# Kernel optimization log

Hardware: AMD Instinct MI355X
Metric: run time of the kernel (lower is better)

## Reference

```python
import jax, jax.numpy as jnp
import numpy as np

HID = 64


def setup_inputs() -> dict:
    key = jax.random.key(0)
    k = jax.random.split(key, 7)
    B, T = 4096, 8192
    x = jax.random.normal(k[0], (B, T, 1), dtype=jnp.float32)
    # Kaiming-uniform-ish init scale; exact values irrelevant for correctness baseline
    W_in = jax.random.normal(k[1], (1, HID), dtype=jnp.float32) * 0.5
    b_in = jax.random.normal(k[2], (HID,), dtype=jnp.float32) * 0.1
    W_s = jax.random.normal(k[3], (HID, HID), dtype=jnp.float32) * (1.0 / np.sqrt(HID))
    b_s = jax.random.normal(k[4], (HID,), dtype=jnp.float32) * 0.1
    W_out = jax.random.normal(k[5], (HID, 1), dtype=jnp.float32) * (1.0 / np.sqrt(HID))
    b_out = jax.random.normal(k[6], (1,), dtype=jnp.float32) * 0.1
    return {"x": x, "W_in": W_in, "b_in": b_in, "W_s": W_s, "b_s": b_s,
            "W_out": W_out, "b_out": b_out}


def reference(x, W_in, b_in, W_s, b_s, W_out, b_out):
    B, T, _ = x.shape
    xt = jnp.swapaxes(x, 0, 1)  # [T, B, 1] -> scan over time

    def step(h, x_t):
        # input_proj on [B,1] -> [B,HID]; tiny GEMM per step (the recurrence is sequential)
        inp = x_t @ W_in + b_in
        h = jax.nn.gelu(h @ W_s + b_s + inp, approximate=False)  # torch GELU = exact erf
        return h, None

    h0 = jnp.zeros((B, HID), dtype=x.dtype)
    h_final, _ = jax.lax.scan(step, h0, xt)
    return h_final @ W_out + b_out  # [B, 1]
```

## Files before the change

### kernel.cpp

```cpp
#include <hip/hip_runtime.h>
#include <cstdint>
#include <cstddef>

#define HID 64
#define RPG 16
#define HSTR 72
#define XSTR 68

typedef short bf16x8 __attribute__((ext_vector_type(8)));
typedef float f32x4 __attribute__((ext_vector_type(4)));

__device__ __forceinline__ float fast_gelu(float z) {
    float u = z * 0.70710678118654752f;
    float a = __builtin_fabsf(u);
    float t = __builtin_amdgcn_rcpf(__builtin_fmaf(0.3275911f, a, 1.0f));
    float e = __builtin_amdgcn_exp2f((u * u) * -1.44269504088896f);
    float p =                   1.061405429f;
    p = __builtin_fmaf(p, t, -1.453152027f);
    p = __builtin_fmaf(p, t,  1.421413741f);
    p = __builtin_fmaf(p, t, -0.284496736f);
    p = __builtin_fmaf(p, t,  0.254829592f);
    p = p * t;
    float er = __builtin_fmaf(-p, e, 1.0f);
    er = __builtin_copysignf(er, u);
    float zh = 0.5f * z;
    return __builtin_fmaf(zh, er, zh);
}

__device__ __forceinline__ ushort bf16_hi(float f) {
    return (ushort)(__float_as_uint(f) >> 16);
}
__device__ __forceinline__ float bf16_f(ushort u) {
    return __uint_as_float(((unsigned)u) << 16);
}

#define STEP(RHI, RLO, WHI, WLO, XB, E0, E1) { \
    const bf16x8 Hhi0 = *reinterpret_cast<const bf16x8*>(RHI); \
    const bf16x8 Hhi1 = *reinterpret_cast<const bf16x8*>((RHI) + 32); \
    const bf16x8 Hlo0 = *reinterpret_cast<const bf16x8*>(RLO); \
    const bf16x8 Hlo1 = *reinterpret_cast<const bf16x8*>((RLO) + 32); \
    const f32x4 zz = {0.f, 0.f, 0.f, 0.f}; \
    f32x4 ahh = __builtin_amdgcn_mfma_f32_16x16x32_bf16(Whi0, Hhi0, zz, 0, 0, 0); \
    f32x4 ac1 = __builtin_amdgcn_mfma_f32_16x16x32_bf16(Whi0, Hlo0, zz, 0, 0, 0); \
    f32x4 ac2 = __builtin_amdgcn_mfma_f32_16x16x32_bf16(Wlo0, Hhi0, zz, 0, 0, 0); \
    ahh = __builtin_amdgcn_mfma_f32_16x16x32_bf16(Whi1, Hhi1, ahh, 0, 0, 0); \
    ac1 = __builtin_amdgcn_mfma_f32_16x16x32_bf16(Whi1, Hlo1, ac1, 0, 0, 0); \
    ac2 = __builtin_amdgcn_mfma_f32_16x16x32_bf16(Wlo1, Hhi1, ac2, 0, 0, 0); \
    const float z0 = (ahh[E0] + ac1[E0]) + (ac2[E0] + __builtin_fmaf((XB), win0, cb0)); \
    const float z1 = (ahh[E1] + ac1[E1]) + (ac2[E1] + __builtin_fmaf((XB), win1, cb1)); \
    const float h0 = fast_gelu(z0); \
    const float h1 = fast_gelu(z1); \
    const unsigned hb0 = __float_as_uint(h0), hb1 = __float_as_uint(h1); \
    *(WHI) = (hb0 >> 16) | (hb1 & 0xffff0000u); \
    const float l0 = h0 - __uint_as_float(hb0 & 0xffff0000u); \
    const float l1 = h1 - __uint_as_float(hb1 & 0xffff0000u); \
    *(WLO) = (__float_as_uint(l0) >> 16) | (__float_as_uint(l1) & 0xffff0000u); \
    __syncthreads(); }

#define MAINLOOP(E0, E1) { \
    const float win0 = W_in[cq + E0]; \
    const float win1 = W_in[cq + E1]; \
    const float cb0  = b_in[cq + E0] + b_s[cq + E0]; \
    const float cb1  = b_in[cq + E1] + b_s[cq + E1]; \
    const ushort* const rhiA = &hlds[0][0][rr * HSTR + 8 * q]; \
    const ushort* const rloA = &hlds[0][1][rr * HSTR + 8 * q]; \
    const ushort* const rhiB = &hlds[1][0][rr * HSTR + 8 * q]; \
    const ushort* const rloB = &hlds[1][1][rr * HSTR + 8 * q]; \
    unsigned* const whiA = reinterpret_cast<unsigned*>(&hlds[0][0][rr * HSTR + cq + E0]); \
    unsigned* const wloA = reinterpret_cast<unsigned*>(&hlds[0][1][rr * HSTR + cq + E0]); \
    unsigned* const whiB = reinterpret_cast<unsigned*>(&hlds[1][0][rr * HSTR + cq + E0]); \
    unsigned* const wloB = reinterpret_cast<unsigned*>(&hlds[1][1][rr * HSTR + cq + E0]); \
    for (int tc = 0; tc < nch; ++tc) { \
        const size_t tg = (size_t)tc * 64; \
        xlds[ww][lane]     = x[(size_t)(bA + ww) * (size_t)T + tg + lane]; \
        xlds[ww + 8][lane] = x[(size_t)(bA + ww + 8) * (size_t)T + tg + lane]; \
        __syncthreads(); \
        _Pragma("unroll 1") \
        for (int t4 = 0; t4 < 16; ++t4) { \
            const f32x4 xq = *reinterpret_cast<const f32x4*>(&xlds[rr][t4 * 4]); \
            STEP(rhiA, rloA, whiB, wloB, xq[0], E0, E1) \
            STEP(rhiB, rloB, whiA, wloA, xq[1], E0, E1) \
            STEP(rhiA, rloA, whiB, wloB, xq[2], E0, E1) \
            STEP(rhiB, rloB, whiA, wloA, xq[3], E0, E1) \
        } \
    } }

__global__ __launch_bounds__(512, 2)
void ssm_kernel(const float* __restrict__ x,
                const float* __restrict__ W_in,
                const float* __restrict__ b_in,
                const float* __restrict__ W_s,
                const float* __restrict__ b_s,
                const float* __restrict__ W_out,
                const float* __restrict__ b_out,
                float* __restrict__ out,
                int B, int T) {
    __shared__ ushort hlds[2][2][RPG * HSTR];
    __shared__ float  xlds[RPG][XSTR];

    const int tid  = threadIdx.x;
    const int ww   = tid >> 6;
    const int g    = ww & 3;
    const int hf   = ww >> 2;
    const int lane = tid & 63;
    const int q    = lane >> 4;
    const int rr   = lane & 15;
    const int bA   = blockIdx.x * RPG;
    const int cq   = 16 * g + 4 * q;

    bf16x8 Whi0, Whi1, Wlo0, Wlo1;
    const int wcol = 16 * g + rr;
#pragma unroll
    for (int e = 0; e < 8; ++e) {
        {   const float wf = W_s[(8 * q + e) * HID + wcol];
            const ushort hi = bf16_hi(wf);
            Whi0[e] = (short)hi;
            Wlo0[e] = (short)bf16_hi(wf - bf16_f(hi)); }
        {   const float wf = W_s[(32 + 8 * q + e) * HID + wcol];
            const ushort hi = bf16_hi(wf);
            Whi1[e] = (short)hi;
            Wlo1[e] = (short)bf16_hi(wf - bf16_f(hi)); }
    }
    asm volatile("" : "+v"(Whi0), "+v"(Whi1), "+v"(Wlo0), "+v"(Wlo1));

    {
        ushort* p = &hlds[0][0][0];
        for (int i = tid; i < 2 * RPG * HSTR; i += 512) p[i] = 0;
    }

    const int nch = T >> 6;

    if (hf == 0) { MAINLOOP(0, 1) } else { MAINLOOP(2, 3) }

    if (ww == 0) {
        const int r  = lane >> 2;
        const int p4 = lane & 3;
        const ushort* hp = &hlds[0][0][r * HSTR + p4 * 16];
        const ushort* lp = &hlds[0][1][r * HSTR + p4 * 16];
        float s = 0.f;
#pragma unroll
        for (int j = 0; j < 16; ++j)
            s = __builtin_fmaf(bf16_f(hp[j]) + bf16_f(lp[j]), W_out[p4 * 16 + j], s);
        s += __shfl_xor(s, 1, 64);
        s += __shfl_xor(s, 2, 64);
        if (p4 == 0) out[bA + r] = s + b_out[0];
    }
}

extern "C" void kernel_launch(void* const* d_in, const int* in_sizes, int n_in,
                              void* d_out, int out_size, void* d_ws, size_t ws_size,
                              hipStream_t stream) {
    const float* x     = (const float*)d_in[0];
    const float* W_in  = (const float*)d_in[1];
    const float* b_in  = (const float*)d_in[2];
    const float* W_s   = (const float*)d_in[3];
    const float* b_s   = (const float*)d_in[4];
    const float* W_out = (const float*)d_in[5];
    const float* b_out = (const float*)d_in[6];
    float* out = (float*)d_out;

    const int B = out_size;
    const int T = in_sizes[0] / B;

    const int blocks = B / RPG;
    ssm_kernel<<<blocks, 512, 0, stream>>>(
        x, W_in, b_in, W_s, b_s, W_out, b_out, out, B, T);
}
```

Baseline: 2.641 ms.

## Halve block to 256 threads, each wave computes four outputs per MFMA tile

Removes the duplicated MFMA work in which two half-blocks each computed the same 16x16 tile but kept only two of its four outputs. Each of four waves now consumes all four accumulator elements, packs them with v_perm, and writes 64-bit LDS stores. The x tile is loaded with float4 and the GELU exponent is rescaled to save a multiply. This cuts redundant matrix work and the number of waves per barrier, but doubles the GELU work per thread and may reduce occupancy and latency hiding.

```diff
diff --git a/kernel.cpp b/kernel.cpp
--- a/kernel.cpp
+++ b/kernel.cpp
@@ -14,7 +14,8 @@
     float u = z * 0.70710678118654752f;
     float a = __builtin_fabsf(u);
     float t = __builtin_amdgcn_rcpf(__builtin_fmaf(0.3275911f, a, 1.0f));
-    float e = __builtin_amdgcn_exp2f((u * u) * -1.44269504088896f);
+    float s = u * 1.20112240878645f;
+    float e = __builtin_amdgcn_exp2f(-(s * s));
     float p =                   1.061405429f;
     p = __builtin_fmaf(p, t, -1.453152027f);
     p = __builtin_fmaf(p, t,  1.421413741f);
@@ -34,7 +35,9 @@
     return __uint_as_float(((unsigned)u) << 16);
 }
 
-#define STEP(RHI, RLO, WHI, WLO, XB, E0, E1) { \
+#define PKHI(b_, a_) __builtin_amdgcn_perm((b_), (a_), 0x07060302u)
+
+#define STEP(RHI, RLO, WHI, WLO, XB) { \
     const bf16x8 Hhi0 = *reinterpret_cast<const bf16x8*>(RHI); \
     const bf16x8 Hhi1 = *reinterpret_cast<const bf16x8*>((RHI) + 32); \
     const bf16x8 Hlo0 = *reinterpret_cast<const bf16x8*>(RLO); \
@@ -46,46 +49,27 @@
     ahh = __builtin_amdgcn_mfma_f32_16x16x32_bf16(Whi1, Hhi1, ahh, 0, 0, 0); \
     ac1 = __builtin_amdgcn_mfma_f32_16x16x32_bf16(Whi1, Hlo1, ac1, 0, 0, 0); \
     ac2 = __builtin_amdgcn_mfma_f32_16x16x32_bf16(Wlo1, Hhi1, ac2, 0, 0, 0); \
-    const float z0 = (ahh[E0] + ac1[E0]) + (ac2[E0] + __builtin_fmaf((XB), win0, cb0)); \
-    const float z1 = (ahh[E1] + ac1[E1]) + (ac2[E1] + __builtin_fmaf((XB), win1, cb1)); \
+    const float z0 = (ahh[0] + ac1[0]) + (ac2[0] + __builtin_fmaf((XB), win0, cb0)); \
+    const float z1 = (ahh[1] + ac1[1]) + (ac2[1] + __builtin_fmaf((XB), win1, cb1)); \
+    const float z2 = (ahh[2] + ac1[2]) + (ac2[2] + __builtin_fmaf((XB), win2, cb2)); \
+    const float z3 = (ahh[3] + ac1[3]) + (ac2[3] + __builtin_fmaf((XB), win3, cb3)); \
     const float h0 = fast_gelu(z0); \
     const float h1 = fast_gelu(z1); \
+    const float h2 = fast_gelu(z2); \
+    const float h3 = fast_gelu(z3); \
     const unsigned hb0 = __float_as_uint(h0), hb1 = __float_as_uint(h1); \
-    *(WHI) = (hb0 >> 16) | (hb1 & 0xffff0000u); \
-    const float l0 = h0 - __uint_as_float(hb0 & 0xffff0000u); \
-    const float l1 = h1 - __uint_as_float(hb1 & 0xffff0000u); \
-    *(WLO) = (__float_as_uint(l0) >> 16) | (__float_as_uint(l1) & 0xffff0000u); \
+    const unsigned hb2 = __float_as_uint(h2), hb3 = __float_as_uint(h3); \
+    uint2 hpk; hpk.x = PKHI(hb1, hb0); hpk.y = PKHI(hb3, hb2); \
+    *(WHI) = hpk; \
+    const unsigned lb0 = __float_as_uint(h0 - __uint_as_float(hb0 & 0xffff0000u)); \
+    const unsigned lb1 = __float_as_uint(h1 - __uint_as_float(hb1 & 0xffff0000u)); \
+    const unsigned lb2 = __float_as_uint(h2 - __uint_as_float(hb2 & 0xffff0000u)); \
+    const unsigned lb3 = __float_as_uint(h3 - __uint_as_float(hb3 & 0xffff0000u)); \
+    uint2 lpk; lpk.x = PKHI(lb1, lb0); lpk.y = PKHI(lb3, lb2); \
+    *(WLO) = lpk; \
     __syncthreads(); }
 
-#define MAINLOOP(E0, E1) { \
-    const float win0 = W_in[cq + E0]; \
-    const float win1 = W_in[cq + E1]; \
-    const float cb0  = b_in[cq + E0] + b_s[cq + E0]; \
-    const float cb1  = b_in[cq + E1] + b_s[cq + E1]; \
-    const ushort* const rhiA = &hlds[0][0][rr * HSTR + 8 * q]; \
-    const ushort* const rloA = &hlds[0][1][rr * HSTR + 8 * q]; \
-    const ushort* const rhiB = &hlds[1][0][rr * HSTR + 8 * q]; \
-    const ushort* const rloB = &hlds[1][1][rr * HSTR + 8 * q]; \
-    unsigned* const whiA = reinterpret_cast<unsigned*>(&hlds[0][0][rr * HSTR + cq + E0]); \
-    unsigned* const wloA = reinterpret_cast<unsigned*>(&hlds[0][1][rr * HSTR + cq + E0]); \
-    unsigned* const whiB = reinterpret_cast<unsigned*>(&hlds[1][0][rr * HSTR + cq + E0]); \
-    unsigned* const wloB = reinterpret_cast<unsigned*>(&hlds[1][1][rr * HSTR + cq + E0]); \
-    for (int tc = 0; tc < nch; ++tc) { \
-        const size_t tg = (size_t)tc * 64; \
-        xlds[ww][lane]     = x[(size_t)(bA + ww) * (size_t)T + tg + lane]; \
-        xlds[ww + 8][lane] = x[(size_t)(bA + ww + 8) * (size_t)T + tg + lane]; \
-        __syncthreads(); \
-        _Pragma("unroll 1") \
-        for (int t4 = 0; t4 < 16; ++t4) { \
-            const f32x4 xq = *reinterpret_cast<const f32x4*>(&xlds[rr][t4 * 4]); \
-            STEP(rhiA, rloA, whiB, wloB, xq[0], E0, E1) \
-            STEP(rhiB, rloB, whiA, wloA, xq[1], E0, E1) \
-            STEP(rhiA, rloA, whiB, wloB, xq[2], E0, E1) \
-            STEP(rhiB, rloB, whiA, wloA, xq[3], E0, E1) \
-        } \
-    } }
-
-__global__ __launch_bounds__(512, 2)
+__global__ __launch_bounds__(256, 1)
 void ssm_kernel(const float* __restrict__ x,
                 const float* __restrict__ W_in,
                 const float* __restrict__ b_in,
@@ -99,14 +83,14 @@
     __shared__ float  xlds[RPG][XSTR];
 
     const int tid  = threadIdx.x;
-    const int ww   = tid >> 6;
-    const int g    = ww & 3;
-    const int hf   = ww >> 2;
+    const int g    = tid >> 6;
     const int lane = tid & 63;
     const int q    = lane >> 4;
     const int rr   = lane & 15;
     const int bA   = blockIdx.x * RPG;
     const int cq   = 16 * g + 4 * q;
+
+    if (bA >= B) return;
 
     bf16x8 Whi0, Whi1, Wlo0, Wlo1;
     const int wcol = 16 * g + rr;
@@ -123,16 +107,50 @@
     }
     asm volatile("" : "+v"(Whi0), "+v"(Whi1), "+v"(Wlo0), "+v"(Wlo1));
 
+    const float win0 = W_in[cq + 0], win1 = W_in[cq + 1];
+    const float win2 = W_in[cq + 2], win3 = W_in[cq + 3];
+    const float cb0 = b_in[cq + 0] + b_s[cq + 0];
+    const float cb1 = b_in[cq + 1] + b_s[cq + 1];
+    const float cb2 = b_in[cq + 2] + b_s[cq + 2];
+    const float cb3 = b_in[cq + 3] + b_s[cq + 3];
+
     {
         ushort* p = &hlds[0][0][0];
-        for (int i = tid; i < 2 * RPG * HSTR; i += 512) p[i] = 0;
+        for (int i = tid; i < 2 * RPG * HSTR; i += 256) p[i] = 0;
     }
+
+    const ushort* const rhiA = &hlds[0][0][rr * HSTR + 8 * q];
+    const ushort* const rloA = &hlds[0][1][rr * HSTR + 8 * q];
+    const ushort* const rhiB = &hlds[1][0][rr * HSTR + 8 * q];
+    const ushort* const rloB = &hlds[1][1][rr * HSTR + 8 * q];
+    uint2* const whiA = reinterpret_cast<uint2*>(&hlds[0][0][rr * HSTR + cq]);
+    uint2* const wloA = reinterpret_cast<uint2*>(&hlds[0][1][rr * HSTR + cq]);
+    uint2* const whiB = reinterpret_cast<uint2*>(&hlds[1][0][rr * HSTR + cq]);
+    uint2* const wloB = reinterpret_cast<uint2*>(&hlds[1][1][rr * HSTR + cq]);
 
     const int nch = T >> 6;
 
-    if (hf == 0) { MAINLOOP(0, 1) } else { MAINLOOP(2, 3) }
+    for (int tc = 0; tc < nch; ++tc) {
+        {
+            const int row = tid >> 4;
+            const int ch  = tid & 15;
+            const float4 xg = *reinterpret_cast<const float4*>(
+                &x[(size_t)(bA + row) * (size_t)T + (size_t)(tc * 64 + ch * 4)]);
+            *reinterpret_cast<float4*>(&xlds[row][ch * 4]) = xg;
+        }
+        __syncthreads();
 
-    if (ww == 0) {
+#pragma unroll 1
+        for (int t4 = 0; t4 < 16; ++t4) {
+            const f32x4 xq = *reinterpret_cast<const f32x4*>(&xlds[rr][t4 * 4]);
+            STEP(rhiA, rloA, whiB, wloB, xq[0])
+            STEP(rhiB, rloB, whiA, wloA, xq[1])
+            STEP(rhiA, rloA, whiB, wloB, xq[2])
+            STEP(rhiB, rloB, whiA, wloA, xq[3])
+        }
+    }
+
+    if (g == 0) {
         const int r  = lane >> 2;
         const int p4 = lane & 3;
         const ushort* hp = &hlds[0][0][r * HSTR + p4 * 16];
@@ -163,6 +181,6 @@
     const int T = in_sizes[0] / B;
 
     const int blocks = B / RPG;
-    ssm_kernel<<<blocks, 512, 0, stream>>>(
+    ssm_kernel<<<blocks, 256, 0, stream>>>(
         x, W_in, b_in, W_s, b_s, W_out, b_out, out, B, T);
 }
```

After: 2.896 ms. 9.6% more time.

## Split recurrent matvec K across wave halves and exchange partial sums through LDS

Applied to the files above, without the earlier changes.

Each pair of waves now splits the 64-wide reduction of the hidden-state matvec. Each wave issues three MFMAs over its 32-element K half instead of six chained MFMAs over the full K. The partial sums are swapped through a new LDS buffer, which adds one extra __syncthreads per time step. The input projection and bias are folded into the MFMA accumulator, bf16 hi/lo packing uses v_perm, and x is loaded as float2. The intent is to shorten the serial per-step dependency chain, at the cost of doubling barriers per step.

```diff
diff --git a/kernel.cpp b/kernel.cpp
--- a/kernel.cpp
+++ b/kernel.cpp
@@ -14,7 +14,8 @@
     float u = z * 0.70710678118654752f;
     float a = __builtin_fabsf(u);
     float t = __builtin_amdgcn_rcpf(__builtin_fmaf(0.3275911f, a, 1.0f));
-    float e = __builtin_amdgcn_exp2f((u * u) * -1.44269504088896f);
+    float s = u * 1.20112240878645f;
+    float e = __builtin_amdgcn_exp2f(-(s * s));
     float p =                   1.061405429f;
     p = __builtin_fmaf(p, t, -1.453152027f);
     p = __builtin_fmaf(p, t,  1.421413741f);
@@ -34,54 +35,53 @@
     return __uint_as_float(((unsigned)u) << 16);
 }
 
-#define STEP(RHI, RLO, WHI, WLO, XB, E0, E1) { \
-    const bf16x8 Hhi0 = *reinterpret_cast<const bf16x8*>(RHI); \
-    const bf16x8 Hhi1 = *reinterpret_cast<const bf16x8*>((RHI) + 32); \
-    const bf16x8 Hlo0 = *reinterpret_cast<const bf16x8*>(RLO); \
-    const bf16x8 Hlo1 = *reinterpret_cast<const bf16x8*>((RLO) + 32); \
+#define PKHI(b_, a_) __builtin_amdgcn_perm((b_), (a_), 0x07060302u)
+
+#define STEP(RHI, RLO, WHI, WLO, XB, BIASED, K0, K1, S0, S1) { \
+    const bf16x8 Hhi = *reinterpret_cast<const bf16x8*>(RHI); \
+    const bf16x8 Hlo = *reinterpret_cast<const bf16x8*>(RLO); \
+    f32x4 ci; \
+    ci[0] = (BIASED) ? __builtin_fmaf((XB), win0, cb0) : 0.f; \
+    ci[1] = (BIASED) ? __builtin_fmaf((XB), win1, cb1) : 0.f; \
+    ci[2] = (BIASED) ? __builtin_fmaf((XB), win2, cb2) : 0.f; \
+    ci[3] = (BIASED) ? __builtin_fmaf((XB), win3, cb3) : 0.f; \
     const f32x4 zz = {0.f, 0.f, 0.f, 0.f}; \
-    f32x4 ahh = __builtin_amdgcn_mfma_f32_16x16x32_bf16(Whi0, Hhi0, zz, 0, 0, 0); \
-    f32x4 ac1 = __builtin_amdgcn_mfma_f32_16x16x32_bf16(Whi0, Hlo0, zz, 0, 0, 0); \
-    f32x4 ac2 = __builtin_amdgcn_mfma_f32_16x16x32_bf16(Wlo0, Hhi0, zz, 0, 0, 0); \
-    ahh = __builtin_amdgcn_mfma_f32_16x16x32_bf16(Whi1, Hhi1, ahh, 0, 0, 0); \
-    ac1 = __builtin_amdgcn_mfma_f32_16x16x32_bf16(Whi1, Hlo1, ac1, 0, 0, 0); \
-    ac2 = __builtin_amdgcn_mfma_f32_16x16x32_bf16(Wlo1, Hhi1, ac2, 0, 0, 0); \
-    const float z0 = (ahh[E0] + ac1[E0]) + (ac2[E0] + __builtin_fmaf((XB), win0, cb0)); \
-    const float z1 = (ahh[E1] + ac1[E1]) + (ac2[E1] + __builtin_fmaf((XB), win1, cb1)); \
+    const f32x4 ahh = __builtin_amdgcn_mfma_f32_16x16x32_bf16(Whi, Hhi, ci, 0, 0, 0); \
+    const f32x4 ac1 = __builtin_amdgcn_mfma_f32_16x16x32_bf16(Whi, Hlo, zz, 0, 0, 0); \
+    const f32x4 ac2 = __builtin_amdgcn_mfma_f32_16x16x32_bf16(Wlo, Hhi, zz, 0, 0, 0); \
+    const f32x4 ps = (ahh + ac1) + ac2; \
+    float2 snd; snd.x = ps[S0]; snd.y = ps[S1]; \
+    *xw = snd; \
+    __syncthreads(); \
+    const float2 rc = *xr; \
+    const float z0 = ps[K0] + rc.x; \
+    const float z1 = ps[K1] + rc.y; \
     const float h0 = fast_gelu(z0); \
     const float h1 = fast_gelu(z1); \
     const unsigned hb0 = __float_as_uint(h0), hb1 = __float_as_uint(h1); \
-    *(WHI) = (hb0 >> 16) | (hb1 & 0xffff0000u); \
-    const float l0 = h0 - __uint_as_float(hb0 & 0xffff0000u); \
-    const float l1 = h1 - __uint_as_float(hb1 & 0xffff0000u); \
-    *(WLO) = (__float_as_uint(l0) >> 16) | (__float_as_uint(l1) & 0xffff0000u); \
+    *(WHI) = PKHI(hb1, hb0); \
+    const unsigned lb0 = __float_as_uint(h0 - __uint_as_float(hb0 & 0xffff0000u)); \
+    const unsigned lb1 = __float_as_uint(h1 - __uint_as_float(hb1 & 0xffff0000u)); \
+    *(WLO) = PKHI(lb1, lb0); \
     __syncthreads(); }
 
-#define MAINLOOP(E0, E1) { \
-    const float win0 = W_in[cq + E0]; \
-    const float win1 = W_in[cq + E1]; \
-    const float cb0  = b_in[cq + E0] + b_s[cq + E0]; \
-    const float cb1  = b_in[cq + E1] + b_s[cq + E1]; \
-    const ushort* const rhiA = &hlds[0][0][rr * HSTR + 8 * q]; \
-    const ushort* const rloA = &hlds[0][1][rr * HSTR + 8 * q]; \
-    const ushort* const rhiB = &hlds[1][0][rr * HSTR + 8 * q]; \
-    const ushort* const rloB = &hlds[1][1][rr * HSTR + 8 * q]; \
-    unsigned* const whiA = reinterpret_cast<unsigned*>(&hlds[0][0][rr * HSTR + cq + E0]); \
-    unsigned* const wloA = reinterpret_cast<unsigned*>(&hlds[0][1][rr * HSTR + cq + E0]); \
-    unsigned* const whiB = reinterpret_cast<unsigned*>(&hlds[1][0][rr * HSTR + cq + E0]); \
-    unsigned* const wloB = reinterpret_cast<unsigned*>(&hlds[1][1][rr * HSTR + cq + E0]); \
+#define MAINLOOP(BIASED, K0, K1, S0, S1) { \
     for (int tc = 0; tc < nch; ++tc) { \
-        const size_t tg = (size_t)tc * 64; \
-        xlds[ww][lane]     = x[(size_t)(bA + ww) * (size_t)T + tg + lane]; \
-        xlds[ww + 8][lane] = x[(size_t)(bA + ww + 8) * (size_t)T + tg + lane]; \
+        { \
+            const int row = tid >> 5;         \
+            const int ch  = tid & 31;         \
+            const float2 xg = *reinterpret_cast<const float2*>( \
+                &x[(size_t)(bA + row) * (size_t)T + (size_t)(tc * 64 + ch * 2)]); \
+            *reinterpret_cast<float2*>(&xlds[row][ch * 2]) = xg; \
+        } \
         __syncthreads(); \
         _Pragma("unroll 1") \
         for (int t4 = 0; t4 < 16; ++t4) { \
             const f32x4 xq = *reinterpret_cast<const f32x4*>(&xlds[rr][t4 * 4]); \
-            STEP(rhiA, rloA, whiB, wloB, xq[0], E0, E1) \
-            STEP(rhiB, rloB, whiA, wloA, xq[1], E0, E1) \
-            STEP(rhiA, rloA, whiB, wloB, xq[2], E0, E1) \
-            STEP(rhiB, rloB, whiA, wloA, xq[3], E0, E1) \
+            STEP(rhiA, rloA, whiB, wloB, xq[0], BIASED, K0, K1, S0, S1) \
+            STEP(rhiB, rloB, whiA, wloA, xq[1], BIASED, K0, K1, S0, S1) \
+            STEP(rhiA, rloA, whiB, wloB, xq[2], BIASED, K0, K1, S0, S1) \
+            STEP(rhiB, rloB, whiA, wloA, xq[3], BIASED, K0, K1, S0, S1) \
         } \
     } }
 
@@ -97,6 +97,7 @@
                 int B, int T) {
     __shared__ ushort hlds[2][2][RPG * HSTR];
     __shared__ float  xlds[RPG][XSTR];
+    __shared__ float  xch[8][64][2];
 
     const int tid  = threadIdx.x;
     const int ww   = tid >> 6;
@@ -108,29 +109,45 @@
     const int bA   = blockIdx.x * RPG;
     const int cq   = 16 * g + 4 * q;
 
-    bf16x8 Whi0, Whi1, Wlo0, Wlo1;
+    if (bA >= B) return;
+
+    bf16x8 Whi, Wlo;
     const int wcol = 16 * g + rr;
 #pragma unroll
     for (int e = 0; e < 8; ++e) {
-        {   const float wf = W_s[(8 * q + e) * HID + wcol];
-            const ushort hi = bf16_hi(wf);
-            Whi0[e] = (short)hi;
-            Wlo0[e] = (short)bf16_hi(wf - bf16_f(hi)); }
-        {   const float wf = W_s[(32 + 8 * q + e) * HID + wcol];
-            const ushort hi = bf16_hi(wf);
-            Whi1[e] = (short)hi;
-            Wlo1[e] = (short)bf16_hi(wf - bf16_f(hi)); }
+        const float wf = W_s[(32 * hf + 8 * q + e) * HID + wcol];
+        const ushort hi = bf16_hi(wf);
+        Whi[e] = (short)hi;
+        Wlo[e] = (short)bf16_hi(wf - bf16_f(hi));
     }
-    asm volatile("" : "+v"(Whi0), "+v"(Whi1), "+v"(Wlo0), "+v"(Wlo1));
+    asm volatile("" : "+v"(Whi), "+v"(Wlo));
+
+    const float win0 = W_in[cq + 0], win1 = W_in[cq + 1];
+    const float win2 = W_in[cq + 2], win3 = W_in[cq + 3];
+    const float cb0 = b_in[cq + 0] + b_s[cq + 0];
+    const float cb1 = b_in[cq + 1] + b_s[cq + 1];
+    const float cb2 = b_in[cq + 2] + b_s[cq + 2];
+    const float cb3 = b_in[cq + 3] + b_s[cq + 3];
 
     {
         ushort* p = &hlds[0][0][0];
-        for (int i = tid; i < 2 * RPG * HSTR; i += 512) p[i] = 0;
+        for (int i = tid; i < 2 * 2 * RPG * HSTR; i += 512) p[i] = 0;
     }
+
+    const ushort* const rhiA = &hlds[0][0][rr * HSTR + 32 * hf + 8 * q];
+    const ushort* const rloA = &hlds[0][1][rr * HSTR + 32 * hf + 8 * q];
+    const ushort* const rhiB = &hlds[1][0][rr * HSTR + 32 * hf + 8 * q];
+    const ushort* const rloB = &hlds[1][1][rr * HSTR + 32 * hf + 8 * q];
+    unsigned* const whiA = reinterpret_cast<unsigned*>(&hlds[0][0][rr * HSTR + cq + 2 * hf]);
+    unsigned* const wloA = reinterpret_cast<unsigned*>(&hlds[0][1][rr * HSTR + cq + 2 * hf]);
+    unsigned* const whiB = reinterpret_cast<unsigned*>(&hlds[1][0][rr * HSTR + cq + 2 * hf]);
+    unsigned* const wloB = reinterpret_cast<unsigned*>(&hlds[1][1][rr * HSTR + cq + 2 * hf]);
+    float2* const xw = reinterpret_cast<float2*>(&xch[ww][lane][0]);
+    const float2* const xr = reinterpret_cast<const float2*>(&xch[ww ^ 4][lane][0]);
 
     const int nch = T >> 6;
 
-    if (hf == 0) { MAINLOOP(0, 1) } else { MAINLOOP(2, 3) }
+    if (hf == 0) { MAINLOOP(1, 0, 1, 2, 3) } else { MAINLOOP(0, 2, 3, 0, 1) }
 
     if (ww == 0) {
         const int r  = lane >> 2;
```

New measurement: 3.090 ms. 1.17x slower.

## Interleave hi/lo hidden rows with XOR swizzle and fold input term into MFMA

Applied to the files above, without the earlier changes.

Changes the LDS hidden-state layout so that each row stores hi and lo bf16 halves contiguously (144 ushorts per row), with XOR-swizzled 8-element slots to avoid bank conflicts on the MFMA operand reads and the packed writes. The input projection plus bias is now passed as the MFMA accumulator init rather than added afterwards. The bf16 packing uses v_perm, the x chunk load uses float2, and the GELU exp2 argument is computed with one fewer multiply. The aim is fewer LDS bank conflicts and fewer VALU ops in the serial per-step critical path, at the cost of extra index arithmetic for the swizzle.

```diff
diff --git a/kernel.cpp b/kernel.cpp
--- a/kernel.cpp
+++ b/kernel.cpp
@@ -4,7 +4,7 @@
 
 #define HID 64
 #define RPG 16
-#define HSTR 72
+#define ROWU 144
 #define XSTR 68
 
 typedef short bf16x8 __attribute__((ext_vector_type(8)));
@@ -14,7 +14,8 @@
     float u = z * 0.70710678118654752f;
     float a = __builtin_fabsf(u);
     float t = __builtin_amdgcn_rcpf(__builtin_fmaf(0.3275911f, a, 1.0f));
-    float e = __builtin_amdgcn_exp2f((u * u) * -1.44269504088896f);
+    float s = u * 1.20112240878645f;
+    float e = __builtin_amdgcn_exp2f(-(s * s));
     float p =                   1.061405429f;
     p = __builtin_fmaf(p, t, -1.453152027f);
     p = __builtin_fmaf(p, t,  1.421413741f);
@@ -34,27 +35,32 @@
     return __uint_as_float(((unsigned)u) << 16);
 }
 
-#define STEP(RHI, RLO, WHI, WLO, XB, E0, E1) { \
-    const bf16x8 Hhi0 = *reinterpret_cast<const bf16x8*>(RHI); \
-    const bf16x8 Hhi1 = *reinterpret_cast<const bf16x8*>((RHI) + 32); \
-    const bf16x8 Hlo0 = *reinterpret_cast<const bf16x8*>(RLO); \
-    const bf16x8 Hlo1 = *reinterpret_cast<const bf16x8*>((RLO) + 32); \
+#define PKHI(b_, a_) __builtin_amdgcn_perm((b_), (a_), 0x07060302u)
+
+#define STEP(RA0, RA1, WHI, WLO, XB, E0, E1) { \
+    const bf16x8 Hhi0 = *reinterpret_cast<const bf16x8*>(RA0); \
+    const bf16x8 Hlo0 = *reinterpret_cast<const bf16x8*>((RA0) + 64); \
+    const bf16x8 Hhi1 = *reinterpret_cast<const bf16x8*>(RA1); \
+    const bf16x8 Hlo1 = *reinterpret_cast<const bf16x8*>((RA1) + 64); \
+    f32x4 ci = {0.f, 0.f, 0.f, 0.f}; \
+    ci[E0] = __builtin_fmaf((XB), win0, cb0); \
+    ci[E1] = __builtin_fmaf((XB), win1, cb1); \
     const f32x4 zz = {0.f, 0.f, 0.f, 0.f}; \
     f32x4 ahh = __builtin_amdgcn_mfma_f32_16x16x32_bf16(Whi0, Hhi0, zz, 0, 0, 0); \
-    f32x4 ac1 = __builtin_amdgcn_mfma_f32_16x16x32_bf16(Whi0, Hlo0, zz, 0, 0, 0); \
+    f32x4 ac1 = __builtin_amdgcn_mfma_f32_16x16x32_bf16(Whi0, Hlo0, ci, 0, 0, 0); \
     f32x4 ac2 = __builtin_amdgcn_mfma_f32_16x16x32_bf16(Wlo0, Hhi0, zz, 0, 0, 0); \
     ahh = __builtin_amdgcn_mfma_f32_16x16x32_bf16(Whi1, Hhi1, ahh, 0, 0, 0); \
     ac1 = __builtin_amdgcn_mfma_f32_16x16x32_bf16(Whi1, Hlo1, ac1, 0, 0, 0); \
     ac2 = __builtin_amdgcn_mfma_f32_16x16x32_bf16(Wlo1, Hhi1, ac2, 0, 0, 0); \
-    const float z0 = (ahh[E0] + ac1[E0]) + (ac2[E0] + __builtin_fmaf((XB), win0, cb0)); \
-    const float z1 = (ahh[E1] + ac1[E1]) + (ac2[E1] + __builtin_fmaf((XB), win1, cb1)); \
+    const float z0 = (ahh[E0] + ac1[E0]) + ac2[E0]; \
+    const float z1 = (ahh[E1] + ac1[E1]) + ac2[E1]; \
     const float h0 = fast_gelu(z0); \
     const float h1 = fast_gelu(z1); \
     const unsigned hb0 = __float_as_uint(h0), hb1 = __float_as_uint(h1); \
-    *(WHI) = (hb0 >> 16) | (hb1 & 0xffff0000u); \
-    const float l0 = h0 - __uint_as_float(hb0 & 0xffff0000u); \
-    const float l1 = h1 - __uint_as_float(hb1 & 0xffff0000u); \
-    *(WLO) = (__float_as_uint(l0) >> 16) | (__float_as_uint(l1) & 0xffff0000u); \
+    *(WHI) = PKHI(hb1, hb0); \
+    const unsigned lb0 = __float_as_uint(h0 - __uint_as_float(hb0 & 0xffff0000u)); \
+    const unsigned lb1 = __float_as_uint(h1 - __uint_as_float(hb1 & 0xffff0000u)); \
+    *(WLO) = PKHI(lb1, lb0); \
     __syncthreads(); }
 
 #define MAINLOOP(E0, E1) { \
@@ -62,26 +68,23 @@
     const float win1 = W_in[cq + E1]; \
     const float cb0  = b_in[cq + E0] + b_s[cq + E0]; \
     const float cb1  = b_in[cq + E1] + b_s[cq + E1]; \
-    const ushort* const rhiA = &hlds[0][0][rr * HSTR + 8 * q]; \
-    const ushort* const rloA = &hlds[0][1][rr * HSTR + 8 * q]; \
-    const ushort* const rhiB = &hlds[1][0][rr * HSTR + 8 * q]; \
-    const ushort* const rloB = &hlds[1][1][rr * HSTR + 8 * q]; \
-    unsigned* const whiA = reinterpret_cast<unsigned*>(&hlds[0][0][rr * HSTR + cq + E0]); \
-    unsigned* const wloA = reinterpret_cast<unsigned*>(&hlds[0][1][rr * HSTR + cq + E0]); \
-    unsigned* const whiB = reinterpret_cast<unsigned*>(&hlds[1][0][rr * HSTR + cq + E0]); \
-    unsigned* const wloB = reinterpret_cast<unsigned*>(&hlds[1][1][rr * HSTR + cq + E0]); \
     for (int tc = 0; tc < nch; ++tc) { \
         const size_t tg = (size_t)tc * 64; \
-        xlds[ww][lane]     = x[(size_t)(bA + ww) * (size_t)T + tg + lane]; \
-        xlds[ww + 8][lane] = x[(size_t)(bA + ww + 8) * (size_t)T + tg + lane]; \
+        { \
+            const int row = tid >> 5;         \
+            const int ch  = tid & 31;         \
+            const float2 xg = *reinterpret_cast<const float2*>( \
+                &x[(size_t)(bA + row) * (size_t)T + tg + ch * 2]); \
+            *reinterpret_cast<float2*>(&xlds[row][ch * 2]) = xg; \
+        } \
         __syncthreads(); \
         _Pragma("unroll 1") \
         for (int t4 = 0; t4 < 16; ++t4) { \
             const f32x4 xq = *reinterpret_cast<const f32x4*>(&xlds[rr][t4 * 4]); \
-            STEP(rhiA, rloA, whiB, wloB, xq[0], E0, E1) \
-            STEP(rhiB, rloB, whiA, wloA, xq[1], E0, E1) \
-            STEP(rhiA, rloA, whiB, wloB, xq[2], E0, E1) \
-            STEP(rhiB, rloB, whiA, wloA, xq[3], E0, E1) \
+            STEP(rA0, rA1, whiB, wloB, xq[0], E0, E1) \
+            STEP(rB0, rB1, whiA, wloA, xq[1], E0, E1) \
+            STEP(rA0, rA1, whiB, wloB, xq[2], E0, E1) \
+            STEP(rB0, rB1, whiA, wloA, xq[3], E0, E1) \
         } \
     } }
 
@@ -95,7 +98,7 @@
                 const float* __restrict__ b_out,
                 float* __restrict__ out,
                 int B, int T) {
-    __shared__ ushort hlds[2][2][RPG * HSTR];
+    __shared__ ushort hlds[2][RPG * ROWU];
     __shared__ float  xlds[RPG][XSTR];
 
     const int tid  = threadIdx.x;
@@ -107,6 +110,8 @@
     const int rr   = lane & 15;
     const int bA   = blockIdx.x * RPG;
     const int cq   = 16 * g + 4 * q;
+
+    if (bA >= B) return;
 
     bf16x8 Whi0, Whi1, Wlo0, Wlo1;
     const int wcol = 16 * g + rr;
@@ -124,9 +129,24 @@
     asm volatile("" : "+v"(Whi0), "+v"(Whi1), "+v"(Wlo0), "+v"(Wlo1));
 
     {
-        ushort* p = &hlds[0][0][0];
-        for (int i = tid; i < 2 * RPG * HSTR; i += 512) p[i] = 0;
+        ushort* p = &hlds[0][0];
+        for (int i = tid; i < 2 * RPG * ROWU; i += 512) p[i] = 0;
     }
+
+    const int sx = (rr & 7) ^ ((rr >> 3) * 5);
+
+    const ushort* const rA0 = &hlds[0][rr * ROWU + 8 * (q ^ sx)];
+    const ushort* const rA1 = &hlds[0][rr * ROWU + 8 * ((q ^ 4) ^ sx)];
+    const ushort* const rB0 = &hlds[1][rr * ROWU + 8 * (q ^ sx)];
+    const ushort* const rB1 = &hlds[1][rr * ROWU + 8 * ((q ^ 4) ^ sx)];
+
+    const int c0  = cq + 2 * hf;
+    const int wl  = c0 >> 3;
+    const int win_idx = rr * ROWU + 8 * (wl ^ sx) + (c0 & 7);
+    unsigned* const whiA = reinterpret_cast<unsigned*>(&hlds[0][win_idx]);
+    unsigned* const wloA = reinterpret_cast<unsigned*>(&hlds[0][win_idx + 64]);
+    unsigned* const whiB = reinterpret_cast<unsigned*>(&hlds[1][win_idx]);
+    unsigned* const wloB = reinterpret_cast<unsigned*>(&hlds[1][win_idx + 64]);
 
     const int nch = T >> 6;
 
@@ -135,12 +155,19 @@
     if (ww == 0) {
         const int r  = lane >> 2;
         const int p4 = lane & 3;
-        const ushort* hp = &hlds[0][0][r * HSTR + p4 * 16];
-        const ushort* lp = &hlds[0][1][r * HSTR + p4 * 16];
+        const int sxr = (r & 7) ^ ((r >> 3) * 5);
         float s = 0.f;
 #pragma unroll
-        for (int j = 0; j < 16; ++j)
-            s = __builtin_fmaf(bf16_f(hp[j]) + bf16_f(lp[j]), W_out[p4 * 16 + j], s);
+        for (int half = 0; half < 2; ++half) {
+            const int slot = 2 * p4 + half;
+            const ushort* hp = &hlds[0][r * ROWU + 8 * (slot ^ sxr)];
+            const ushort* lp = hp + 64;
+#pragma unroll
+            for (int j = 0; j < 8; ++j) {
+                const float hv = bf16_f(hp[j]) + bf16_f(lp[j]);
+                s = __builtin_fmaf(hv, W_out[8 * slot + j], s);
+            }
+        }
         s += __shfl_xor(s, 1, 64);
         s += __shfl_xor(s, 2, 64);
         if (p4 == 0) out[bA + r] = s + b_out[0];
```

Result: faster. 2.580 ms (-2.3%).
